# Optimization experiments

Hardware: AMD Instinct MI355X
Metric: run time of the kernel (lower is better)

Reference implementation:

```python
import jax, jax.numpy as jnp
import numpy as np
import math

D = 2048  # hidden_size
B, S = 4, 2048
EPS = 1e-5


def _ln(z, g, b):
    m = jnp.mean(z, axis=-1, keepdims=True)
    v = jnp.mean(jnp.square(z - m), axis=-1, keepdims=True)
    return (z - m) * jax.lax.rsqrt(v + EPS) * g + b


def _rotate_half(x):
    h = x.shape[-1] // 2
    return jnp.concatenate([-x[..., h:], x[..., :h]], axis=-1)


def _mas_normalize(logits):
    m = jnp.max(jnp.abs(logits), axis=-1, keepdims=True)
    return logits / (m + 1e-9)


def setup_inputs() -> dict:
    key = jax.random.key(0)
    ks = jax.random.split(key, 12)
    std = 0.02
    return {
        "x": jax.random.normal(ks[0], (B, S, D), dtype=jnp.float32),
        "position_ids": jnp.arange(S, dtype=jnp.int32),
        "ln1_g": jnp.ones((D,), jnp.float32),
        "ln1_b": jnp.zeros((D,), jnp.float32),
        # stacked params for [q, k, v, o]
        "mu_w": std * jax.random.normal(ks[1], (4, D, D), dtype=jnp.float32),
        "mu_b": jnp.zeros((4, D), jnp.float32),
        "proto_w": std * jax.random.normal(ks[2], (4, D, D), dtype=jnp.float32),
        "gate": jnp.zeros((4, D), jnp.float32),
        "pt_w": std * jax.random.normal(ks[3], (4, D, D), dtype=jnp.float32),
        "pln_g": jnp.ones((4, D), jnp.float32),
        "pln_b": jnp.zeros((4, D), jnp.float32),
        "incoming": std * jax.random.normal(ks[4], (4, D, D), dtype=jnp.float32),
    }


def reference(x, position_ids, ln1_g, ln1_b, mu_w, mu_b, proto_w, gate,
              pt_w, pln_g, pln_b, incoming):
    d = x.shape[-1]
    inv_sqrt_d = 1.0 / math.sqrt(d)

    # proto_state = proto_weight + LN(Linear(incoming))  per module [4, D, D]
    prc = jnp.einsum('nij,noj->nio', incoming, pt_w)
    proto_state = proto_w + _ln(prc, pln_g[:, None, :], pln_b[:, None, :])

    ln1_out = _ln(x, ln1_g, ln1_b)            # [B,S,D]
    ctx = jnp.mean(ln1_out, axis=1)           # [B,D]

    # qkv computation outputs: silu(ln1_out @ mu_w.T + mu_b) for n in {q,k,v}
    comp = jax.nn.silu(jnp.einsum('bsd,nod->nbso', ln1_out, mu_w[:3])
                       + mu_b[:3][:, None, None, :])            # [3,B,S,D]
    # routing from context vector
    match_ctx = jnp.einsum('bd,nod->nbo', ctx, proto_state[:3]) * inv_sqrt_d
    routing = match_ctx + gate[:3][:, None, :]                  # [3,B,D]
    gating = _mas_normalize(routing)
    masked = gating[:, :, None, :] * comp                       # [3,B,S,D]
    q, k, v = masked[0], masked[1], masked[2]

    # RoPE over full hidden dim (num_heads == 1)
    seq = position_ids.shape[0]
    inv_freq = 1.0 / (10000.0 ** (jnp.arange(0, d, 2, dtype=jnp.float32) / d))
    t = jnp.arange(seq, dtype=jnp.float32)
    freqs = t[:, None] * inv_freq[None, :]
    emb = jnp.concatenate([freqs, freqs], axis=-1)              # [S,D]
    cos = jnp.cos(emb)[position_ids]
    sin = jnp.sin(emb)[position_ids]
    q = q * cos + _rotate_half(q) * sin
    k = k * cos + _rotate_half(k) * sin

    # causal single-head attention, scale 1/sqrt(head_dim=D)
    scores = jnp.einsum('bqd,bkd->bqk', q, k) * inv_sqrt_d      # [B,S,S]
    causal = jnp.tril(jnp.ones((seq, seq), dtype=bool))
    scores = jnp.where(causal, scores, jnp.finfo(scores.dtype).min)
    probs = jax.nn.softmax(scores, axis=-1)
    attn_out = jnp.einsum('bqk,bkd->bqd', probs, v)             # [B,S,D]

    # output SPL + routing
    ctx_o = jnp.mean(attn_out, axis=1)
    c_o = jax.nn.silu(jnp.einsum('bsd,od->bso', attn_out, mu_w[3]) + mu_b[3])
    match_o = jnp.einsum('bd,od->bo', ctx_o, proto_state[3]) * inv_sqrt_d
    gating_o = _mas_normalize(match_o + gate[3])
    x_out = x + gating_o[:, None, :] * c_o
    return x_out
```

## Files before the change

### kernel.cpp

```cpp
#include <hip/hip_runtime.h>
#include <hip/hip_bf16.h>
#include <hip/hip_fp16.h>

#define Dh 2048
#define Bh 4
#define Sh 2048
#define NROW 8192
#define HALF 1024
#define INV_SQRT_D 0.022097086912079608f
#define LNEPS 1e-5f

typedef __hip_bfloat16 bf16;
typedef short short8 __attribute__((ext_vector_type(8)));
typedef float f32x4 __attribute__((ext_vector_type(4)));
typedef unsigned short ushort8v __attribute__((ext_vector_type(8)));
typedef unsigned short ushort4v __attribute__((ext_vector_type(4)));

__device__ inline float h2f_bits(unsigned short u) {
  __half h;
  *(unsigned short*)&h = u;
  return __half2float(h);
}
__device__ inline unsigned short bf_bits(float f) {
  bf16 t = __float2bfloat16(f);
  return *(unsigned short*)&t;
}

__device__ inline float warp_sum(float x) {
#pragma unroll
  for (int o = 32; o > 0; o >>= 1) x += __shfl_down(x, o);
  return x;
}
__device__ inline float warp_max(float x) {
#pragma unroll
  for (int o = 32; o > 0; o >>= 1) x = fmaxf(x, __shfl_down(x, o));
  return x;
}
__device__ inline float block_sum(float x, float* sm4) {
  x = warp_sum(x);
  int w = threadIdx.x >> 6;
  if ((threadIdx.x & 63) == 0) sm4[w] = x;
  __syncthreads();
  float r = sm4[0] + sm4[1] + sm4[2] + sm4[3];
  __syncthreads();
  return r;
}
__device__ inline float block_max(float x, float* sm4) {
  x = warp_max(x);
  int w = threadIdx.x >> 6;
  if ((threadIdx.x & 63) == 0) sm4[w] = x;
  __syncthreads();
  float r = fmaxf(fmaxf(sm4[0], sm4[1]), fmaxf(sm4[2], sm4[3]));
  __syncthreads();
  return r;
}

__device__ inline void gload_lds16(const void* g, void* lds) {
  __builtin_amdgcn_global_load_lds(
      (const __attribute__((address_space(1))) unsigned int*)(unsigned long long)g,
      (__attribute__((address_space(3))) unsigned int*)(unsigned long long)lds,
      16, 0, 0);
}

#define MM4(R, AF, B0, B1, B2, B3)                                             \
  acc[R][0] = __builtin_amdgcn_mfma_f32_16x16x32_bf16(AF, B0, acc[R][0], 0, 0, 0); \
  acc[R][1] = __builtin_amdgcn_mfma_f32_16x16x32_bf16(AF, B1, acc[R][1], 0, 0, 0); \
  acc[R][2] = __builtin_amdgcn_mfma_f32_16x16x32_bf16(AF, B2, acc[R][2], 0, 0, 0); \
  acc[R][3] = __builtin_amdgcn_mfma_f32_16x16x32_bf16(AF, B3, acc[R][3], 0, 0, 0);

template <int MODE>
__global__ __launch_bounds__(512) void pgemm(
    const bf16* __restrict__ Aall, const bf16* __restrict__ Ball,
    void* __restrict__ Call, int N, int K, int lda, int ldb,
    long sAz, long sBz, long sCz,
    const float* __restrict__ e0, const float* __restrict__ e1,
    const float* __restrict__ e2, bf16* __restrict__ vt) {
  const int bm0 = blockIdx.x * 256;
  const int bn0 = blockIdx.y * 256;
  if (MODE == 2 && bn0 > bm0 + 255) return;
  const int z = blockIdx.z;
  const bf16* A = Aall + (long)z * sAz;
  const bf16* B = Ball + (long)z * sBz;

  __shared__ __align__(16) char smem[163840];
  const int tid = threadIdx.x;
  const int l = tid & 63, w = tid >> 6;
  const int wr = w >> 2, wc = w & 3;

  f32x4 acc[8][4] = {};
  const int nt = K >> 6;

  const int sg = (((l & 7) ^ ((l >> 3) & 7)) << 3);
  const int srow = (w << 3) + (l >> 3);
  const bf16* aS0 = A + (long)(bm0 + srow) * lda + sg;
  const bf16* aS1 = A + (long)(bm0 + 64 + srow) * lda + sg;
  const bf16* aS2 = A + (long)(bm0 + 128 + srow) * lda + sg;
  const bf16* aS3 = A + (long)(bm0 + 192 + srow) * lda + sg;
  const bf16* bT0 = B + (long)(bn0 + srow) * ldb + sg;
  const bf16* bT1 = B + (long)(bn0 + 64 + srow) * ldb + sg;
  const bf16* bT2 = B + (long)(bn0 + 128 + srow) * ldb + sg;
  const bf16* bT3 = B + (long)(bn0 + 192 + srow) * ldb + sg;
  char* const dA = smem + (w << 10);
  char* const dB = smem + 65536 + (w << 10);

  auto stageA = [&](int tt) {
    int boff = (tt & 1) << 15;
    gload_lds16(aS0 + (tt << 6), dA + boff);
    gload_lds16(aS1 + (tt << 6), dA + boff + 8192);
    gload_lds16(aS2 + (tt << 6), dA + boff + 16384);
    gload_lds16(aS3 + (tt << 6), dA + boff + 24576);
  };
  auto stageB = [&](int tt) {
    int boff = (tt % 3) << 15;
    gload_lds16(bT0 + (tt << 6), dB + boff);
    gload_lds16(bT1 + (tt << 6), dB + boff + 8192);
    gload_lds16(bT2 + (tt << 6), dB + boff + 16384);
    gload_lds16(bT3 + (tt << 6), dB + boff + 24576);
  };

  stageA(0); stageB(0);
  if (nt > 1) stageB(1);
  if (nt > 1) asm volatile("s_waitcnt vmcnt(4)" ::: "memory");
  else        asm volatile("s_waitcnt vmcnt(0)" ::: "memory");
  __builtin_amdgcn_sched_barrier(0);
  asm volatile("s_barrier" ::: "memory");

  const int rslot = (((l >> 4) ^ (l & 7)) << 4);
  const int abyte = (((wr << 7) + (l & 15)) << 7) + rslot;
  const int bbyte = (((wc << 6) + (l & 15)) << 7) + rslot;

  for (int t = 0; t < nt; ++t) {
    const char* Ab = smem + ((t & 1) << 15);
    const char* Bb = smem + 65536 + ((t % 3) << 15);
    short8 b00 = *(const short8*)(Bb + bbyte);
    short8 b01 = *(const short8*)(Bb + bbyte + 2048);
    short8 b02 = *(const short8*)(Bb + bbyte + 4096);
    short8 b03 = *(const short8*)(Bb + bbyte + 6144);
    short8 b10 = *(const short8*)(Bb + (bbyte ^ 64));
    short8 b11 = *(const short8*)(Bb + ((bbyte + 2048) ^ 64));
    short8 b12 = *(const short8*)(Bb + ((bbyte + 4096) ^ 64));
    short8 b13 = *(const short8*)(Bb + ((bbyte + 6144) ^ 64));
    short8 a0 = *(const short8*)(Ab + abyte);
    short8 a1 = *(const short8*)(Ab + abyte + 2048);
    short8 a2 = *(const short8*)(Ab + abyte + 4096);
    short8 a3 = *(const short8*)(Ab + abyte + 6144);
    short8 a4 = *(const short8*)(Ab + abyte + 8192);
    short8 a5 = *(const short8*)(Ab + abyte + 10240);
    short8 a6 = *(const short8*)(Ab + abyte + 12288);
    short8 a7 = *(const short8*)(Ab + abyte + 14336);
    if (t + 1 < nt) stageA(t + 1);
    MM4(0, a0, b00, b01, b02, b03) MM4(1, a1, b00, b01, b02, b03)
    MM4(2, a2, b00, b01, b02, b03) MM4(3, a3, b00, b01, b02, b03)
    MM4(4, a4, b00, b01, b02, b03) MM4(5, a5, b00, b01, b02, b03)
    MM4(6, a6, b00, b01, b02, b03) MM4(7, a7, b00, b01, b02, b03)
    short8 c0 = *(const short8*)(Ab + (abyte ^ 64));
    short8 c1 = *(const short8*)(Ab + ((abyte + 2048) ^ 64));
    short8 c2 = *(const short8*)(Ab + ((abyte + 4096) ^ 64));
    short8 c3 = *(const short8*)(Ab + ((abyte + 6144) ^ 64));
    short8 c4 = *(const short8*)(Ab + ((abyte + 8192) ^ 64));
    short8 c5 = *(const short8*)(Ab + ((abyte + 10240) ^ 64));
    short8 c6 = *(const short8*)(Ab + ((abyte + 12288) ^ 64));
    short8 c7 = *(const short8*)(Ab + ((abyte + 14336) ^ 64));
    if (t + 2 < nt) stageB(t + 2);
    MM4(0, c0, b10, b11, b12, b13) MM4(1, c1, b10, b11, b12, b13)
    MM4(2, c2, b10, b11, b12, b13) MM4(3, c3, b10, b11, b12, b13)
    MM4(4, c4, b10, b11, b12, b13) MM4(5, c5, b10, b11, b12, b13)
    MM4(6, c6, b10, b11, b12, b13) MM4(7, c7, b10, b11, b12, b13)
    if (t < nt - 1) {
      asm volatile("s_waitcnt lgkmcnt(0)" ::: "memory");
      if (t + 2 < nt) asm volatile("s_waitcnt vmcnt(4)" ::: "memory");
      else            asm volatile("s_waitcnt vmcnt(0)" ::: "memory");
      __builtin_amdgcn_sched_barrier(0);
      asm volatile("s_barrier" ::: "memory");
    }
  }

  const int lc = l & 15, lr4 = (l >> 4) << 2;
  if (MODE == 1 && z == 2) {
    unsigned short* tl = (unsigned short*)smem;
    const int bb = bm0 >> 11, s0r = bm0 & 2047;
    __syncthreads();
#pragma unroll
    for (int fr = 0; fr < 8; ++fr) {
      int row0 = (wr << 7) + fr * 16 + lr4;
#pragma unroll
      for (int fc = 0; fc < 4; ++fc) {
        int col = (wc << 6) + fc * 16 + lc;
        int gc = bn0 + col;
        ushort4v u;
#pragma unroll
        for (int qv = 0; qv < 4; ++qv) {
          float val = acc[fr][fc][qv] + e0[2 * Dh + gc];
          float sil = val / (1.f + __expf(-val));
          u[qv] = bf_bits(sil * e1[(2 * Bh + bb) * Dh + gc]);
        }
        *(ushort4v*)(tl + col * 264 + row0) = u;
      }
    }
    __syncthreads();
#pragma unroll
    for (int it = 0; it < 4; ++it) {
      int idx = tid + it * 512;
      int col = idx >> 3, ch = idx & 7;
      const ushort8v* src = (const ushort8v*)(tl + col * 264 + ch * 32);
      ushort8v v0 = src[0], v1 = src[1], v2 = src[2], v3 = src[3];
      ushort8v* dst = (ushort8v*)((unsigned short*)vt +
          ((long)bb * Dh + bn0 + col) * Sh + s0r + ch * 32);
      dst[0] = v0; dst[1] = v1; dst[2] = v2; dst[3] = v3;
    }
  } else {
#pragma unroll
    for (int fr = 0; fr < 8; ++fr) {
      int gr0 = bm0 + (wr << 7) + fr * 16 + lr4;
#pragma unroll
      for (int fc = 0; fc < 4; ++fc) {
        int gc = bn0 + (wc << 6) + fc * 16 + lc;
#pragma unroll
        for (int qv = 0; qv < 4; ++qv) {
          int gr = gr0 + qv;
          float a = acc[fr][fc][qv];
          if (MODE == 0) {
            ((bf16*)Call + (long)z * sCz)[(long)gr * N + gc] =
                __float2bfloat16(a);
          } else if (MODE == 1) {
            float val = a + e0[z * Dh + gc];
            float sil = val / (1.f + __expf(-val));
            int bb = gr >> 11;
            float g = e1[(z * Bh + bb) * Dh + gc];
            ((bf16*)Call + (long)z * sCz)[(long)gr * N + gc] =
                __float2bfloat16(sil * g);
          } else if (MODE == 2) {
            ((__half*)Call + (long)z * sCz)[(long)gr * N + gc] =
                __float2half(a * INV_SQRT_D);
          } else {
            float val = a + e0[gc];
            float sil = val / (1.f + __expf(-val));
            int bb = gr >> 11;
            ((float*)Call)[(long)gr * N + gc] =
                e2[(long)gr * N + gc] + e1[bb * Dh + gc] * sil;
          }
        }
      }
    }
  }
}

__global__ __launch_bounds__(512) void pgemm_h(
    const bf16* __restrict__ Aall, const bf16* __restrict__ Ball,
    bf16* __restrict__ Call, int N, int lda, int ldb,
    long sAz, long sBz, long sCz) {
  const int fid = blockIdx.x;
  const int p = fid >> 8, q = fid & 255;
  const int mh = q >> 5;
  const int z = (q >> 3) & 3, ni = q & 7;
  const int mi = p ? (15 - mh) : mh;
  const int bm0 = mi * 128, bn0 = ni * 256;
  const bf16* A = Aall + (long)z * sAz;
  const bf16* B = Ball + (long)z * sBz;

  __shared__ __align__(16) char smem[131072];
  const int tid = threadIdx.x;
  const int l = tid & 63, w = tid >> 6;
  const int wr = w >> 2, wc = w & 3;
  f32x4 acc[4][4] = {};
  const int nt = (bm0 + 128) >> 6;

  const int sg = (((l & 7) ^ ((l >> 3) & 7)) << 3);
  const int srow = (w << 3) + (l >> 3);
  const bf16* aS0 = A + (long)(bm0 + srow) * lda + sg;
  const bf16* aS1 = A + (long)(bm0 + 64 + srow) * lda + sg;
  const bf16* bT0 = B + (long)(bn0 + srow) * ldb + sg;
  const bf16* bT1 = B + (long)(bn0 + 64 + srow) * ldb + sg;
  const bf16* bT2 = B + (long)(bn0 + 128 + srow) * ldb + sg;
  const bf16* bT3 = B + (long)(bn0 + 192 + srow) * ldb + sg;
  char* const dA = smem + (w << 10);
  char* const dB = smem + 32768 + (w << 10);

  auto stageA = [&](int tt) {
    int boff = (tt & 1) << 14;
    gload_lds16(aS0 + (tt << 6), dA + boff);
    gload_lds16(aS1 + (tt << 6), dA + boff + 8192);
  };
  auto stageB = [&](int tt) {
    int boff = (tt % 3) << 15;
    gload_lds16(bT0 + (tt << 6), dB + boff);
    gload_lds16(bT1 + (tt << 6), dB + boff + 8192);
    gload_lds16(bT2 + (tt << 6), dB + boff + 16384);
    gload_lds16(bT3 + (tt << 6), dB + boff + 24576);
  };

  stageA(0); stageB(0); stageB(1);
  asm volatile("s_waitcnt vmcnt(4)" ::: "memory");
  __builtin_amdgcn_sched_barrier(0);
  asm volatile("s_barrier" ::: "memory");

  const int rslot = (((l >> 4) ^ (l & 7)) << 4);
  const int abyte = (((wr << 6) + (l & 15)) << 7) + rslot;
  const int bbyte = (((wc << 6) + (l & 15)) << 7) + rslot;

  for (int t = 0; t < nt; ++t) {
    const char* Ab = smem + ((t & 1) << 14);
    const char* Bb = smem + 32768 + ((t % 3) << 15);
    short8 b00 = *(const short8*)(Bb + bbyte);
    short8 b01 = *(const short8*)(Bb + bbyte + 2048);
    short8 b02 = *(const short8*)(Bb + bbyte + 4096);
    short8 b03 = *(const short8*)(Bb + bbyte + 6144);
    short8 b10 = *(const short8*)(Bb + (bbyte ^ 64));
    short8 b11 = *(const short8*)(Bb + ((bbyte + 2048) ^ 64));
    short8 b12 = *(const short8*)(Bb + ((bbyte + 4096) ^ 64));
    short8 b13 = *(const short8*)(Bb + ((bbyte + 6144) ^ 64));
    short8 a0 = *(const short8*)(Ab + abyte);
    short8 a1 = *(const short8*)(Ab + abyte + 2048);
    short8 a2 = *(const short8*)(Ab + abyte + 4096);
    short8 a3 = *(const short8*)(Ab + abyte + 6144);
    if (t + 1 < nt) stageA(t + 1);
    MM4(0, a0, b00, b01, b02, b03) MM4(1, a1, b00, b01, b02, b03)
    MM4(2, a2, b00, b01, b02, b03) MM4(3, a3, b00, b01, b02, b03)
    short8 c0 = *(const short8*)(Ab + (abyte ^ 64));
    short8 c1 = *(const short8*)(Ab + ((abyte + 2048) ^ 64));
    short8 c2 = *(const short8*)(Ab + ((abyte + 4096) ^ 64));
    short8 c3 = *(const short8*)(Ab + ((abyte + 6144) ^ 64));
    if (t + 2 < nt) stageB(t + 2);
    MM4(0, c0, b10, b11, b12, b13) MM4(1, c1, b10, b11, b12, b13)
    MM4(2, c2, b10, b11, b12, b13) MM4(3, c3, b10, b11, b12, b13)
    if (t < nt - 1) {
      asm volatile("s_waitcnt lgkmcnt(0)" ::: "memory");
      if (t + 2 < nt) asm volatile("s_waitcnt vmcnt(4)" ::: "memory");
      else            asm volatile("s_waitcnt vmcnt(0)" ::: "memory");
      __builtin_amdgcn_sched_barrier(0);
      asm volatile("s_barrier" ::: "memory");
    }
  }

  const int lc = l & 15, lr4 = (l >> 4) << 2;
  bf16* C = Call + (long)z * sCz;
#pragma unroll
  for (int fr = 0; fr < 4; ++fr) {
    int gr0 = bm0 + (wr << 6) + fr * 16 + lr4;
#pragma unroll
    for (int fc = 0; fc < 4; ++fc) {
      int gc = bn0 + (wc << 6) + fc * 16 + lc;
#pragma unroll
      for (int qv = 0; qv < 4; ++qv)
        C[(long)(gr0 + qv) * N + gc] = __float2bfloat16(acc[fr][fc][qv]);
    }
  }
}

__global__ __launch_bounds__(256) void cvt3_kernel(
    const float* __restrict__ s0, const float* __restrict__ s1,
    const float* __restrict__ s2, bf16* __restrict__ o0, bf16* __restrict__ o1,
    bf16* __restrict__ o2, long n) {
  const float* in = (blockIdx.y == 0) ? s0 : (blockIdx.y == 1) ? s1 : s2;
  bf16* out = (blockIdx.y == 0) ? o0 : (blockIdx.y == 1) ? o1 : o2;
  long i = ((long)blockIdx.x * 256 + threadIdx.x) * 4;
  if (i >= n) return;
  float4 v = *(const float4*)(in + i);
  out[i + 0] = __float2bfloat16(v.x);
  out[i + 1] = __float2bfloat16(v.y);
  out[i + 2] = __float2bfloat16(v.z);
  out[i + 3] = __float2bfloat16(v.w);
}

__global__ __launch_bounds__(256) void ln1_kernel(const float* __restrict__ x,
    const float* __restrict__ g, const float* __restrict__ b, bf16* __restrict__ out) {
  __shared__ float sm4[4];
  long r = blockIdx.x;
  const float* row = x + r * Dh;
  int i0 = threadIdx.x * 4, i1 = 1024 + threadIdx.x * 4;
  float4 v0 = *(const float4*)(row + i0);
  float4 v1 = *(const float4*)(row + i1);
  float s = v0.x + v0.y + v0.z + v0.w + v1.x + v1.y + v1.z + v1.w;
  float s2 = v0.x * v0.x + v0.y * v0.y + v0.z * v0.z + v0.w * v0.w +
             v1.x * v1.x + v1.y * v1.y + v1.z * v1.z + v1.w * v1.w;
  s = block_sum(s, sm4);
  s2 = block_sum(s2, sm4);
  float mean = s * (1.f / Dh);
  float rstd = rsqrtf(s2 * (1.f / Dh) - mean * mean + LNEPS);
  float4 g0 = *(const float4*)(g + i0);
  float4 g1 = *(const float4*)(g + i1);
  float4 b0 = *(const float4*)(b + i0);
  float4 b1 = *(const float4*)(b + i1);
  ushort4v u0, u1;
  u0[0] = bf_bits((v0.x - mean) * rstd * g0.x + b0.x);
  u0[1] = bf_bits((v0.y - mean) * rstd * g0.y + b0.y);
  u0[2] = bf_bits((v0.z - mean) * rstd * g0.z + b0.z);
  u0[3] = bf_bits((v0.w - mean) * rstd * g0.w + b0.w);
  u1[0] = bf_bits((v1.x - mean) * rstd * g1.x + b1.x);
  u1[1] = bf_bits((v1.y - mean) * rstd * g1.y + b1.y);
  u1[2] = bf_bits((v1.z - mean) * rstd * g1.z + b1.z);
  u1[3] = bf_bits((v1.w - mean) * rstd * g1.w + b1.w);
  *(ushort4v*)(out + r * Dh + i0) = u0;
  *(ushort4v*)(out + r * Dh + i1) = u1;
}

__global__ __launch_bounds__(256) void meanrow_kernel(const bf16* __restrict__ in,
                                                      float* __restrict__ outbd) {
  int gid = blockIdx.x * 256 + threadIdx.x;
  int s0 = blockIdx.y * 128;
  long base = ((long)(gid >> 11) * Sh + s0) * Dh + (gid & 2047);
  float s = 0.f;
  for (int t = 0; t < 128; ++t) s += __bfloat162float(in[base + (long)t * Dh]);
  atomicAdd(&outbd[gid], s * (1.f / Sh));
}

__global__ __launch_bounds__(256) void route_kernel(
    const bf16* __restrict__ prc, const float* __restrict__ proto_w,
    const float* __restrict__ pln_g, const float* __restrict__ pln_b,
    const float* __restrict__ gate, const float* __restrict__ ctx,
    float* __restrict__ routing, float* __restrict__ ps3) {
  __shared__ float sm4[4];
  int i = blockIdx.x, n = blockIdx.y;
  long rb = ((long)n * Dh + i) * Dh;
  float v[8];
  float s = 0.f, s2 = 0.f;
#pragma unroll
  for (int c = 0; c < 8; ++c) {
    float t = __bfloat162float(prc[rb + threadIdx.x + c * 256]);
    v[c] = t; s += t; s2 += t * t;
  }
  s = block_sum(s, sm4);
  s2 = block_sum(s2, sm4);
  float mean = s * (1.f / Dh);
  float rstd = rsqrtf(s2 * (1.f / Dh) - mean * mean + LNEPS);
  if (n == 3) {
#pragma unroll
    for (int c = 0; c < 8; ++c) {
      int o = threadIdx.x + c * 256;
      float ps = proto_w[rb + o] + (v[c] - mean) * rstd * pln_g[3 * Dh + o] + pln_b[3 * Dh + o];
      ps3[(long)i * Dh + o] = ps;
    }
  } else {
    float acc[4] = {0.f, 0.f, 0.f, 0.f};
#pragma unroll
    for (int c = 0; c < 8; ++c) {
      int o = threadIdx.x + c * 256;
      float ps = proto_w[rb + o] + (v[c] - mean) * rstd * pln_g[n * Dh + o] + pln_b[n * Dh + o];
#pragma unroll
      for (int b = 0; b < 4; ++b) acc[b] += ps * ctx[b * Dh + o];
    }
    for (int b = 0; b < 4; ++b) {
      float r = block_sum(acc[b], sm4);
      if (threadIdx.x == 0)
        routing[(n * 4 + b) * Dh + i] = r * INV_SQRT_D + gate[n * Dh + i];
    }
  }
}

__global__ __launch_bounds__(256) void route_o_kernel(
    const float* __restrict__ ps3, const float* __restrict__ ctxo,
    const float* __restrict__ gate, float* __restrict__ routing) {
  __shared__ float sm4[4];
  int i = blockIdx.x;
  float acc[4] = {0.f, 0.f, 0.f, 0.f};
#pragma unroll
  for (int c = 0; c < 8; ++c) {
    int o = threadIdx.x + c * 256;
    float p = ps3[(long)i * Dh + o];
#pragma unroll
    for (int b = 0; b < 4; ++b) acc[b] += p * ctxo[b * Dh + o];
  }
  for (int b = 0; b < 4; ++b) {
    float r = block_sum(acc[b], sm4);
    if (threadIdx.x == 0)
      routing[(12 + b) * Dh + i] = r * INV_SQRT_D + gate[3 * Dh + i];
  }
}

__global__ __launch_bounds__(256) void masnorm_kernel(const float* __restrict__ rin,
                                                      float* __restrict__ gout) {
  __shared__ float sm4[4];
  long r = blockIdx.x;
  float m = 0.f;
#pragma unroll
  for (int c = 0; c < 8; ++c)
    m = fmaxf(m, fabsf(rin[r * Dh + threadIdx.x + c * 256]));
  m = block_max(m, sm4);
  float inv = 1.f / (m + 1e-9f);
#pragma unroll
  for (int c = 0; c < 8; ++c) {
    int o = threadIdx.x + c * 256;
    gout[r * Dh + o] = rin[r * Dh + o] * inv;
  }
}

__global__ __launch_bounds__(256) void rope_table_kernel(float* __restrict__ cosT,
                                                         float* __restrict__ sinT) {
  int idx = blockIdx.x * 256 + threadIdx.x;
  int t = idx >> 10, f = idx & 1023;
  float inv_freq = expf(-(float)f * (9.210340371976184f / 1024.f));
  float ang = (float)t * inv_freq;
  cosT[idx] = cosf(ang);
  sinT[idx] = sinf(ang);
}

__global__ __launch_bounds__(256) void rope_kernel(bf16* __restrict__ q, bf16* __restrict__ k,
    const int* __restrict__ pos, const float* __restrict__ cosT,
    const float* __restrict__ sinT) {
  long r = blockIdx.x;
  int s = (int)(r & (Sh - 1));
  int p = pos[s];
#pragma unroll
  for (int c = 0; c < 4; ++c) {
    int t = threadIdx.x + c * 256;
    float cv = cosT[(long)p * HALF + t];
    float sv = sinT[(long)p * HALF + t];
    long i1 = r * Dh + t, i2 = i1 + HALF;
    float q1 = __bfloat162float(q[i1]), q2 = __bfloat162float(q[i2]);
    q[i1] = __float2bfloat16(q1 * cv - q2 * sv);
    q[i2] = __float2bfloat16(q2 * cv + q1 * sv);
    float k1 = __bfloat162float(k[i1]), k2 = __bfloat162float(k[i2]);
    k[i1] = __float2bfloat16(k1 * cv - k2 * sv);
    k[i2] = __float2bfloat16(k2 * cv + k1 * sv);
  }
}

__global__ __launch_bounds__(256) void softmax_kernel(const unsigned short* __restrict__ scores,
                                                      bf16* __restrict__ probs) {
  __shared__ float buf[Sh];
  __shared__ float sm4[4];
  long r = blockIdx.x;
  int qi = (int)(r & (Sh - 1));
  const unsigned short* row = scores + r * (long)Sh;
  bf16* prow = probs + r * (long)Sh;
  int tid = threadIdx.x;
  int n = qi + 1, nv = n & ~7;
  float m = -3.0e38f;
  for (int o = tid * 8; o < nv; o += 2048) {
    ushort8v v = *(const ushort8v*)(row + o);
#pragma unroll
    for (int j = 0; j < 8; ++j) {
      float x = h2f_bits(v[j]);
      buf[o + j] = x;
      m = fmaxf(m, x);
    }
  }
  for (int o = nv + tid; o < n; o += 256) {
    float x = h2f_bits(row[o]); buf[o] = x; m = fmaxf(m, x);
  }
  m = block_max(m, sm4);
  float s = 0.f;
  for (int o = tid; o < n; o += 256) {
    float e = __expf(buf[o] - m); buf[o] = e; s += e;
  }
  s = block_sum(s, sm4);
  float inv = 1.f / s;
  for (int o = tid * 8; o < nv; o += 2048) {
    ushort8v u;
#pragma unroll
    for (int j = 0; j < 8; ++j) u[j] = bf_bits(buf[o + j] * inv);
    *(ushort8v*)(prow + o) = u;
  }
  for (int o = nv + tid; o < n; o += 256) prow[o] = __float2bfloat16(buf[o] * inv);
  int za = (n + 7) & ~7;
  for (int o = n + tid; o < za && o < Sh; o += 256) prow[o] = __float2bfloat16(0.f);
  ushort8v zz = {0, 0, 0, 0, 0, 0, 0, 0};
  for (int o = za + tid * 8; o < Sh; o += 2048) *(ushort8v*)(prow + o) = zz;
}

extern "C" void kernel_launch(void* const* d_in, const int* in_sizes, int n_in,
                              void* d_out, int out_size, void* d_ws, size_t ws_size,
                              hipStream_t stream) {
  const float* x       = (const float*)d_in[0];
  const int*   pos     = (const int*)d_in[1];
  const float* ln1_g   = (const float*)d_in[2];
  const float* ln1_b   = (const float*)d_in[3];
  const float* mu_w    = (const float*)d_in[4];
  const float* mu_b    = (const float*)d_in[5];
  const float* proto_w = (const float*)d_in[6];
  const float* gate    = (const float*)d_in[7];
  const float* pt_w    = (const float*)d_in[8];
  const float* pln_g   = (const float*)d_in[9];
  const float* pln_b   = (const float*)d_in[10];
  const float* incoming= (const float*)d_in[11];

  char* w = (char*)d_ws;
  const long BF = 33554432L;
  bf16*  ln1    = (bf16*)(w);
  bf16*  qb     = (bf16*)(w + BF);
  bf16*  kb     = (bf16*)(w + 2 * BF);
  bf16*  vb     = (bf16*)(w + 3 * BF);
  bf16*  attn   = (bf16*)(w + 4 * BF);
  bf16*  mu_wb  = (bf16*)(w + 5 * BF);
  bf16*  ptw_b  = (bf16*)(w + 6 * BF);
  bf16*  vT     = ptw_b;
  bf16*  inc_b  = (bf16*)(w + 7 * BF);
  bf16*  probs  = inc_b;
  float* ps3    = (float*)(w + 8 * BF);
  float* cosT   = (float*)(w + 8 * BF + 16777216L);
  float* sinT   = cosT + (long)Sh * HALF;
  float* ctx    = sinT + (long)Sh * HALF;
  float* ctxo   = ctx + Bh * Dh;
  float* routing= ctxo + Bh * Dh;
  float* gating = routing + 16 * Dh;
  bf16*   prc    = (bf16*)d_out;
  __half* scores = (__half*)d_out;
  (void)vb;

  const long DD4 = 4L * Dh * Dh;

  hipMemsetAsync(ctx, 0, 2L * Bh * Dh * sizeof(float), stream);

  rope_table_kernel<<<(Sh * HALF) / 256, 256, 0, stream>>>(cosT, sinT);
  cvt3_kernel<<<dim3(DD4 / 1024, 3), 256, 0, stream>>>(
      mu_w, incoming, pt_w, mu_wb, inc_b, ptw_b, DD4);
  ln1_kernel<<<NROW, 256, 0, stream>>>(x, ln1_g, ln1_b, ln1);
  meanrow_kernel<<<dim3(32, 16), 256, 0, stream>>>(ln1, ctx);
  pgemm<0><<<dim3(8, 8, 4), 512, 0, stream>>>(
      inc_b, ptw_b, prc, Dh, Dh, Dh, Dh,
      (long)Dh * Dh, (long)Dh * Dh, (long)Dh * Dh,
      nullptr, nullptr, nullptr, nullptr);
  route_kernel<<<dim3(Dh, 4), 256, 0, stream>>>(prc, proto_w, pln_g, pln_b,
                                                gate, ctx, routing, ps3);
  masnorm_kernel<<<12, 256, 0, stream>>>(routing, gating);
  pgemm<1><<<dim3(32, 8, 3), 512, 0, stream>>>(
      ln1, mu_wb, qb, Dh, Dh, Dh, Dh,
      0L, (long)Dh * Dh, (long)NROW * Dh, mu_b, gating, nullptr, vT);
  rope_kernel<<<NROW, 256, 0, stream>>>(qb, kb, pos, cosT, sinT);
  pgemm<2><<<dim3(8, 8, 4), 512, 0, stream>>>(
      qb, kb, scores, Sh, Dh, Dh, Dh,
      (long)Sh * Dh, (long)Sh * Dh, (long)Sh * Sh,
      nullptr, nullptr, nullptr, nullptr);
  softmax_kernel<<<Bh * Sh, 256, 0, stream>>>((const unsigned short*)scores, probs);
  pgemm_h<<<512, 512, 0, stream>>>(
      probs, vT, attn, Dh, Sh, Sh,
      (long)Sh * Sh, (long)Dh * Sh, (long)Sh * Dh);
  meanrow_kernel<<<dim3(32, 16), 256, 0, stream>>>(attn, ctxo);
  route_o_kernel<<<Dh, 256, 0, stream>>>(ps3, ctxo, gate, routing);
  masnorm_kernel<<<4, 256, 0, stream>>>(routing + 12 * Dh, gating + 12 * Dh);
  pgemm<4><<<dim3(32, 8, 1), 512, 0, stream>>>(
      attn, mu_wb + 3L * Dh * Dh, d_out, Dh, Dh, Dh, Dh,
      0L, 0L, 0L, mu_b + 3 * Dh, gating + 12 * Dh, x, nullptr);
}
```

Measured before the change: 601.9 us.

## Fuse fp32-to-bf16 conversion into the proto-state GEMM loads; trim softmax zero-fill

Adds a GEMM variant that stages fp32 incoming and pt_w tiles straight into LDS and converts them to bf16 fragments in registers. This drops the separate conversion pass and the bf16 copies for those two weight tensors, saving a full read/write of 2x64MB. In exchange the tiles take twice the LDS space and the inner loop does extra conversion work. The softmax kernel also zero-fills probs only up to the end of the 128-row causal block rather than the full row, which relies on the PV GEMM never reading beyond that point.

Result: slower. 614.0 us (+2.0%).

```diff
diff --git a/kernel.cpp b/kernel.cpp
--- a/kernel.cpp
+++ b/kernel.cpp
@@ -24,6 +24,14 @@
 __device__ inline unsigned short bf_bits(float f) {
   bf16 t = __float2bfloat16(f);
   return *(unsigned short*)&t;
+}
+__device__ inline short8 cvt8(f32x4 lo, f32x4 hi) {
+  short8 r;
+  r[0] = (short)bf_bits(lo[0]); r[1] = (short)bf_bits(lo[1]);
+  r[2] = (short)bf_bits(lo[2]); r[3] = (short)bf_bits(lo[3]);
+  r[4] = (short)bf_bits(hi[0]); r[5] = (short)bf_bits(hi[1]);
+  r[6] = (short)bf_bits(hi[2]); r[7] = (short)bf_bits(hi[3]);
+  return r;
 }
 
 __device__ inline float warp_sum(float x) {
@@ -219,10 +227,7 @@
         for (int qv = 0; qv < 4; ++qv) {
           int gr = gr0 + qv;
           float a = acc[fr][fc][qv];
-          if (MODE == 0) {
-            ((bf16*)Call + (long)z * sCz)[(long)gr * N + gc] =
-                __float2bfloat16(a);
-          } else if (MODE == 1) {
+          if (MODE == 1) {
             float val = a + e0[z * Dh + gc];
             float sil = val / (1.f + __expf(-val));
             int bb = gr >> 11;
@@ -241,6 +246,111 @@
           }
         }
       }
+    }
+  }
+}
+
+__global__ __launch_bounds__(512) void pgemm_f32(
+    const float* __restrict__ Aall, const float* __restrict__ Ball,
+    bf16* __restrict__ Call, int N, int K, int lda, int ldb,
+    long sAz, long sBz, long sCz) {
+  const int bm0 = blockIdx.x * 256;
+  const int bn0 = blockIdx.y * 256;
+  const int z = blockIdx.z;
+  const float* A = Aall + (long)z * sAz;
+  const float* B = Ball + (long)z * sBz;
+
+  __shared__ __align__(16) char smem[163840];
+  const int tid = threadIdx.x;
+  const int l = tid & 63, w = tid >> 6;
+  const int wr = w >> 2, wc = w & 3;
+
+  f32x4 acc[8][4] = {};
+  const int nt = K >> 5;
+
+  const int sgf = (((l & 7) ^ ((l >> 3) & 7)) << 2);
+  const int srow = (w << 3) + (l >> 3);
+  const float* aS0 = A + (long)(bm0 + srow) * lda + sgf;
+  const float* aS1 = A + (long)(bm0 + 64 + srow) * lda + sgf;
+  const float* aS2 = A + (long)(bm0 + 128 + srow) * lda + sgf;
+  const float* aS3 = A + (long)(bm0 + 192 + srow) * lda + sgf;
+  const float* bT0 = B + (long)(bn0 + srow) * ldb + sgf;
+  const float* bT1 = B + (long)(bn0 + 64 + srow) * ldb + sgf;
+  const float* bT2 = B + (long)(bn0 + 128 + srow) * ldb + sgf;
+  const float* bT3 = B + (long)(bn0 + 192 + srow) * ldb + sgf;
+  char* const dA = smem + (w << 10);
+  char* const dB = smem + 65536 + (w << 10);
+
+  auto stageA = [&](int tt) {
+    int boff = (tt & 1) << 15;
+    gload_lds16(aS0 + (tt << 5), dA + boff);
+    gload_lds16(aS1 + (tt << 5), dA + boff + 8192);
+    gload_lds16(aS2 + (tt << 5), dA + boff + 16384);
+    gload_lds16(aS3 + (tt << 5), dA + boff + 24576);
+  };
+  auto stageB = [&](int tt) {
+    int boff = (tt % 3) << 15;
+    gload_lds16(bT0 + (tt << 5), dB + boff);
+    gload_lds16(bT1 + (tt << 5), dB + boff + 8192);
+    gload_lds16(bT2 + (tt << 5), dB + boff + 16384);
+    gload_lds16(bT3 + (tt << 5), dB + boff + 24576);
+  };
+
+  stageA(0); stageB(0); stageB(1);
+  asm volatile("s_waitcnt vmcnt(4)" ::: "memory");
+  __builtin_amdgcn_sched_barrier(0);
+  asm volatile("s_barrier" ::: "memory");
+
+  const int c7 = l & 7, h2 = (l >> 4) << 1;
+  const int aslot = ((h2 ^ c7) << 4);
+  const int abase = (((wr << 7) + (l & 15)) << 7) + aslot;
+  const int bbase = (((wc << 6) + (l & 15)) << 7) + aslot;
+
+#define FRAG(PTR, OFF) cvt8(*(const f32x4*)((PTR) + (OFF)),                   \
+                            *(const f32x4*)((PTR) + ((OFF) ^ 16)))
+
+  for (int t = 0; t < nt; ++t) {
+    const char* Ab = smem + ((t & 1) << 15);
+    const char* Bb = smem + 65536 + ((t % 3) << 15);
+    short8 b0 = FRAG(Bb, bbase);
+    short8 b1 = FRAG(Bb, bbase + 2048);
+    short8 b2 = FRAG(Bb, bbase + 4096);
+    short8 b3 = FRAG(Bb, bbase + 6144);
+    short8 a0 = FRAG(Ab, abase);
+    short8 a1 = FRAG(Ab, abase + 2048);
+    short8 a2 = FRAG(Ab, abase + 4096);
+    short8 a3 = FRAG(Ab, abase + 6144);
+    if (t + 1 < nt) stageA(t + 1);
+    MM4(0, a0, b0, b1, b2, b3) MM4(1, a1, b0, b1, b2, b3)
+    MM4(2, a2, b0, b1, b2, b3) MM4(3, a3, b0, b1, b2, b3)
+    short8 a4 = FRAG(Ab, abase + 8192);
+    short8 a5 = FRAG(Ab, abase + 10240);
+    short8 a6 = FRAG(Ab, abase + 12288);
+    short8 a7 = FRAG(Ab, abase + 14336);
+    if (t + 2 < nt) stageB(t + 2);
+    MM4(4, a4, b0, b1, b2, b3) MM4(5, a5, b0, b1, b2, b3)
+    MM4(6, a6, b0, b1, b2, b3) MM4(7, a7, b0, b1, b2, b3)
+    if (t < nt - 1) {
+      asm volatile("s_waitcnt lgkmcnt(0)" ::: "memory");
+      if (t + 2 < nt) asm volatile("s_waitcnt vmcnt(4)" ::: "memory");
+      else            asm volatile("s_waitcnt vmcnt(0)" ::: "memory");
+      __builtin_amdgcn_sched_barrier(0);
+      asm volatile("s_barrier" ::: "memory");
+    }
+  }
+#undef FRAG
+
+  const int lc = l & 15, lr4 = (l >> 4) << 2;
+  bf16* C = Call + (long)z * sCz;
+#pragma unroll
+  for (int fr = 0; fr < 8; ++fr) {
+    int gr0 = bm0 + (wr << 7) + fr * 16 + lr4;
+#pragma unroll
+    for (int fc = 0; fc < 4; ++fc) {
+      int gc = bn0 + (wc << 6) + fc * 16 + lc;
+#pragma unroll
+      for (int qv = 0; qv < 4; ++qv)
+        C[(long)(gr0 + qv) * N + gc] = __float2bfloat16(acc[fr][fc][qv]);
     }
   }
 }
@@ -347,12 +457,8 @@
   }
 }
 
-__global__ __launch_bounds__(256) void cvt3_kernel(
-    const float* __restrict__ s0, const float* __restrict__ s1,
-    const float* __restrict__ s2, bf16* __restrict__ o0, bf16* __restrict__ o1,
-    bf16* __restrict__ o2, long n) {
-  const float* in = (blockIdx.y == 0) ? s0 : (blockIdx.y == 1) ? s1 : s2;
-  bf16* out = (blockIdx.y == 0) ? o0 : (blockIdx.y == 1) ? o1 : o2;
+__global__ __launch_bounds__(256) void cvt_kernel(
+    const float* __restrict__ in, bf16* __restrict__ out, long n) {
   long i = ((long)blockIdx.x * 256 + threadIdx.x) * 4;
   if (i >= n) return;
   float4 v = *(const float4*)(in + i);
@@ -552,10 +658,11 @@
     *(ushort8v*)(prow + o) = u;
   }
   for (int o = nv + tid; o < n; o += 256) prow[o] = __float2bfloat16(buf[o] * inv);
+  int zlim = (qi & ~127) + 128;
   int za = (n + 7) & ~7;
-  for (int o = n + tid; o < za && o < Sh; o += 256) prow[o] = __float2bfloat16(0.f);
+  for (int o = n + tid; o < za && o < zlim; o += 256) prow[o] = __float2bfloat16(0.f);
   ushort8v zz = {0, 0, 0, 0, 0, 0, 0, 0};
-  for (int o = za + tid * 8; o < Sh; o += 2048) *(ushort8v*)(prow + o) = zz;
+  for (int o = za + tid * 8; o < zlim; o += 2048) *(ushort8v*)(prow + o) = zz;
 }
 
 extern "C" void kernel_launch(void* const* d_in, const int* in_sizes, int n_in,
@@ -579,13 +686,10 @@
   bf16*  ln1    = (bf16*)(w);
   bf16*  qb     = (bf16*)(w + BF);
   bf16*  kb     = (bf16*)(w + 2 * BF);
-  bf16*  vb     = (bf16*)(w + 3 * BF);
   bf16*  attn   = (bf16*)(w + 4 * BF);
   bf16*  mu_wb  = (bf16*)(w + 5 * BF);
-  bf16*  ptw_b  = (bf16*)(w + 6 * BF);
-  bf16*  vT     = ptw_b;
-  bf16*  inc_b  = (bf16*)(w + 7 * BF);
-  bf16*  probs  = inc_b;
+  bf16*  vT     = (bf16*)(w + 6 * BF);
+  bf16*  probs  = (bf16*)(w + 7 * BF);
   float* ps3    = (float*)(w + 8 * BF);
   float* cosT   = (float*)(w + 8 * BF + 16777216L);
   float* sinT   = cosT + (long)Sh * HALF;
@@ -595,21 +699,18 @@
   float* gating = routing + 16 * Dh;
   bf16*   prc    = (bf16*)d_out;
   __half* scores = (__half*)d_out;
-  (void)vb;
 
   const long DD4 = 4L * Dh * Dh;
 
   hipMemsetAsync(ctx, 0, 2L * Bh * Dh * sizeof(float), stream);
 
   rope_table_kernel<<<(Sh * HALF) / 256, 256, 0, stream>>>(cosT, sinT);
-  cvt3_kernel<<<dim3(DD4 / 1024, 3), 256, 0, stream>>>(
-      mu_w, incoming, pt_w, mu_wb, inc_b, ptw_b, DD4);
+  cvt_kernel<<<DD4 / 1024, 256, 0, stream>>>(mu_w, mu_wb, DD4);
   ln1_kernel<<<NROW, 256, 0, stream>>>(x, ln1_g, ln1_b, ln1);
   meanrow_kernel<<<dim3(32, 16), 256, 0, stream>>>(ln1, ctx);
-  pgemm<0><<<dim3(8, 8, 4), 512, 0, stream>>>(
-      inc_b, ptw_b, prc, Dh, Dh, Dh, Dh,
-      (long)Dh * Dh, (long)Dh * Dh, (long)Dh * Dh,
-      nullptr, nullptr, nullptr, nullptr);
+  pgemm_f32<<<dim3(8, 8, 4), 512, 0, stream>>>(
+      incoming, pt_w, prc, Dh, Dh, Dh, Dh,
+      (long)Dh * Dh, (long)Dh * Dh, (long)Dh * Dh);
   route_kernel<<<dim3(Dh, 4), 256, 0, stream>>>(prc, proto_w, pln_g, pln_b,
                                                 gate, ctx, routing, ps3);
   masnorm_kernel<<<12, 256, 0, stream>>>(routing, gating);
```
